# Kernel optimization log

Hardware: AMD Instinct MI355X
Metric: run time of the kernel (lower is better)

The kernel has to match this reference:

```python
import jax, jax.numpy as jnp
import numpy as np

P, Q = 3, 0
DIM = 1 << (P + Q)  # 8 blades, bitmask-indexed: 1,e1,e2,e3,e12,e13,e23,e123
EPS = 1e-6


def _cayley(p, q):
    """Cayley tensor C[i,j,k]: e_i * e_j = sum_k C[i,j,k] e_k for Cl(p,q)."""
    n = p + q
    dim = 1 << n
    C = np.zeros((dim, dim, dim), dtype=np.float32)
    for a in range(dim):
        for b in range(dim):
            # sign from reordering basis vectors into canonical order
            s = 1
            aa = a >> 1
            while aa:
                if bin(aa & b).count('1') & 1:
                    s = -s
                aa >>= 1
            # metric signs from squared shared basis vectors (negative for q part)
            shared = a & b
            for i in range(n):
                if (shared >> i) & 1 and i >= p:
                    s = -s
            C[a, b, a ^ b] = s
    return jnp.asarray(C)

CAYLEY = _cayley(P, Q)
# reversion sign per blade: (-1)^{g(g-1)/2}, g = grade = popcount(bitmask)
REV = jnp.asarray([(-1.0) ** ((bin(k).count('1') * (bin(k).count('1') - 1)) // 2)
                   for k in range(DIM)], dtype=jnp.float32)

B, CH = 131072, 16


def setup_inputs() -> dict:
    key = jax.random.key(0)
    k1, k2, k3 = jax.random.split(key, 3)
    x = jax.random.normal(k1, (B, CH, DIM), dtype=jnp.float32)
    ln_scale = jnp.ones((CH,), dtype=jnp.float32)
    rotor = jax.random.normal(k2, (CH, DIM), dtype=jnp.float32)
    w = jax.random.normal(k3, (CH, CH, DIM), dtype=jnp.float32) / np.sqrt(CH * DIM)
    bias = jnp.zeros((CH, DIM), dtype=jnp.float32)
    return {"x": x, "ln_scale": ln_scale, "rotor": rotor, "w": w, "bias": bias}


def reference(x, ln_scale, rotor, w, bias):
    # CliffordLayerNorm: normalize each channel's multivector by its blade norm
    n = jnp.sqrt(jnp.sum(x * x, axis=-1, keepdims=True) + EPS)  # [B,C,1]
    x = x / n * ln_scale[None, :, None]
    # RotorLayer: unit rotor per channel, sandwich product R x ~R via Cayley
    r = rotor / jnp.sqrt(jnp.sum(rotor * rotor, axis=-1, keepdims=True) + EPS)  # [C,8]
    r_rev = r * REV[None, :]
    t = jnp.einsum('ci,bcj,ijk->bck', r, x, CAYLEY)      # R * x
    x = jnp.einsum('bci,cj,ijk->bck', t, r_rev, CAYLEY)  # (R*x) * ~R
    # GeometricGELU: per-blade exact GELU
    x = jax.nn.gelu(x, approximate=False)
    # CliffordLinear: multivector-valued weights, geometric-product contraction
    out = jnp.einsum('oci,bcj,ijk->bok', w, x, CAYLEY) + bias[None]
    return out
```

## Files before the change

kernel.cpp:

```cpp
#include <hip/hip_runtime.h>
#include <math.h>
#include <stdint.h>

#define CH 16
#define DIM 8
#define ROW 128
#define TILE_ROWS 64
#define BLK 256

typedef __attribute__((ext_vector_type(8))) short bf16x8;
typedef __attribute__((ext_vector_type(4))) float f32x4;
typedef __attribute__((ext_vector_type(4))) unsigned int u32x4;

__device__ __forceinline__ float csign(int a, int b) {
    int s = 0;
    int aa = a >> 1;
    while (aa) { s ^= (__popc(aa & b) & 1); aa >>= 1; }
    return s ? -1.0f : 1.0f;
}

__device__ __forceinline__ unsigned short f2bf(float f) {
    union { float f; unsigned u; } x; x.f = f;
    unsigned r = x.u + 0x7FFF + ((x.u >> 16) & 1);
    return (unsigned short)(r >> 16);
}

__device__ __forceinline__ float gelu_poly(float s) {
    const float z = s * 0.70710678f;
    const float u = z * z;
    float p = -8.5483270e-04f;
    p = fmaf(p, u,  5.2239776e-03f);
    p = fmaf(p, u, -2.6866138e-02f);
    p = fmaf(p, u,  1.1283792e-01f);
    p = fmaf(p, u, -3.7612639e-01f);
    p = fmaf(p, u,  1.1283792e+00f);
    return 0.5f * s * fmaf(z, p, 1.0f);
}

__device__ __forceinline__ void barrier_lgkm() {
    asm volatile("s_waitcnt lgkmcnt(0)" ::: "memory");
    __builtin_amdgcn_s_barrier();
    __builtin_amdgcn_sched_barrier(0);
}

__global__ void precompute_kernel(const float* __restrict__ rotor,
                                  const float* __restrict__ w,
                                  const float* __restrict__ ln_scale,
                                  float* __restrict__ ws)
{
    const int t = threadIdx.x;
    unsigned short* D   = (unsigned short*)ws;
    unsigned short* w2r = D + 16384;

    if (blockIdx.x == 0) {
        ((u32x4*)D)[t]        = (u32x4){0u, 0u, 0u, 0u};
        ((u32x4*)D)[t + 1024] = (u32x4){0u, 0u, 0u, 0u};
        __syncthreads();

        if (t < CH) {
            const int c = t;
            float r[8];
            float nn = 0.f;
            #pragma unroll
            for (int i = 0; i < 8; ++i) { r[i] = rotor[c * 8 + i]; nn += r[i] * r[i]; }
            const float inv = rsqrtf(nn + 1e-6f);
            #pragma unroll
            for (int i = 0; i < 8; ++i) r[i] *= inv;

            const float REVv[8] = {1.f, 1.f, 1.f, -1.f, 1.f, -1.f, -1.f, -1.f};
            float rr[8];
            #pragma unroll
            for (int j = 0; j < 8; ++j) rr[j] = r[j] * REVv[j];

            float L[8][8], R[8][8];
            #pragma unroll
            for (int a = 0; a < 8; ++a)
                #pragma unroll
                for (int b = 0; b < 8; ++b) { L[a][b] = 0.f; R[a][b] = 0.f; }

            #pragma unroll
            for (int i = 0; i < 8; ++i)
                #pragma unroll
                for (int j = 0; j < 8; ++j) {
                    const float s = csign(i, j);
                    L[i ^ j][j] += r[i] * s;
                    R[i ^ j][i] += rr[j] * s;
                }

            const float sc = ln_scale[c];
            #pragma unroll
            for (int k = 0; k < 8; ++k)
                #pragma unroll
                for (int m = 0; m < 8; ++m) {
                    float acc = 0.f;
                    #pragma unroll
                    for (int i = 0; i < 8; ++i) acc += R[k][i] * L[i][m];
                    D[(c * 8 + k) * ROW + (c * 8 + m)] = f2bf(acc * sc);
                }
        }
    } else {
        #pragma unroll
        for (int task = t; task < ROW * CH; task += 1024) {
            const int outf = task >> 4;
            const int ci   = task & 15;
            const int kb = outf & 7, o = outf >> 3;
            const float4 w0 = *(const float4*)(w + (o * CH + ci) * 8);
            const float4 w1 = *(const float4*)(w + (o * CH + ci) * 8 + 4);
            const float wv[8] = {w0.x, w0.y, w0.z, w0.w, w1.x, w1.y, w1.z, w1.w};
            bf16x8 pk;
            #pragma unroll
            for (int j = 0; j < 8; ++j) {
                const int i = kb ^ j;
                pk[j] = (short)f2bf(wv[i] * csign(i, j));
            }
            *(bf16x8*)(w2r + outf * ROW + ci * 8) = pk;
        }
    }
}


__device__ __forceinline__ void phase1_mv(const float4 a, const float4 b,
                                          const bf16x8* Df, unsigned short* sG,
                                          int wave, int lcol, int lkg, int rt) {
    const float nn = a.x*a.x + a.y*a.y + a.z*a.z + a.w*a.w
                   + b.x*b.x + b.y*b.y + b.z*b.z + b.w*b.w;
    const float inv = rsqrtf(nn + 1e-6f);
    bf16x8 af;
    af[0] = (short)f2bf(a.x * inv); af[1] = (short)f2bf(a.y * inv);
    af[2] = (short)f2bf(a.z * inv); af[3] = (short)f2bf(a.w * inv);
    af[4] = (short)f2bf(b.x * inv); af[5] = (short)f2bf(b.y * inv);
    af[6] = (short)f2bf(b.z * inv); af[7] = (short)f2bf(b.w * inv);

    f32x4 p0 = (f32x4){0.f, 0.f, 0.f, 0.f};
    f32x4 p1 = (f32x4){0.f, 0.f, 0.f, 0.f};
    p0 = __builtin_amdgcn_mfma_f32_16x16x32_bf16(af, Df[0], p0, 0, 0, 0);
    p1 = __builtin_amdgcn_mfma_f32_16x16x32_bf16(af, Df[1], p1, 0, 0, 0);

    #pragma unroll
    for (int ctl = 0; ctl < 2; ++ctl) {
        const f32x4 p = ctl ? p1 : p0;
        const int colg = (2 * wave + ctl) * 16 + lcol;
        #pragma unroll
        for (int j = 0; j < 4; ++j) {
            const float y = gelu_poly(p[j]);
            const int row   = rt * 16 + lkg * 4 + j;
            const int chunk = (colg >> 3) ^ (row & 15);
            sG[row * ROW + chunk * 8 + (colg & 7)] = f2bf(y);
        }
    }
}

__global__ __launch_bounds__(BLK, 4) void fused_kernel(
        const float* __restrict__ x,
        const float* __restrict__ bias,
        const float* __restrict__ ws,
        float* __restrict__ out)
{
    __shared__ unsigned short sG[TILE_ROWS * ROW];

    const int t    = threadIdx.x;
    const int lane = t & 63;
    const int wave = t >> 6;
    const int lcol = lane & 15;
    const int lkg  = lane >> 4;
    const int c    = 4 * wave + lkg;

    const unsigned short* D   = (const unsigned short*)ws;
    const unsigned short* w2r = D + 16384;

    const size_t row0 = (size_t)blockIdx.x * TILE_ROWS;

    float4 xa[4], xb[4];
    #pragma unroll
    for (int rt = 0; rt < 4; ++rt) {
        const float4* xp = (const float4*)(x + ((row0 + rt * 16 + lcol) * CH + c) * DIM);
        xa[rt] = xp[0];
        xb[rt] = xp[1];
    }

    bf16x8 Df[2];
    #pragma unroll
    for (int ctl = 0; ctl < 2; ++ctl) {
        const int col = (2 * wave + ctl) * 16 + lcol;
        Df[ctl] = *(const bf16x8*)(D + col * ROW + 32 * wave + lkg * 8);
    }

    #pragma unroll
    for (int rt = 0; rt < 4; ++rt)
        phase1_mv(xa[rt], xb[rt], Df, sG, wave, lcol, lkg, rt);

    const int colb = wave * 32;
    bf16x8 Bf[2][4];
    #pragma unroll
    for (int ct = 0; ct < 2; ++ct)
        #pragma unroll
        for (int ks = 0; ks < 4; ++ks) {
            const int col = colb + ct * 16 + lcol;
            Bf[ct][ks] = *(const bf16x8*)(w2r + col * ROW + ks * 32 + lkg * 8);
        }
    float bv[2];
    bv[0] = bias[colb + lcol];
    bv[1] = bias[colb + 16 + lcol];

    barrier_lgkm();

    f32x4 acc[4][2];
    #pragma unroll
    for (int rt = 0; rt < 4; ++rt)
        #pragma unroll
        for (int ct = 0; ct < 2; ++ct)
            acc[rt][ct] = (f32x4){0.f, 0.f, 0.f, 0.f};

    #pragma unroll
    for (int rt = 0; rt < 4; ++rt) {
        const int row = rt * 16 + lcol;
        #pragma unroll
        for (int ks = 0; ks < 4; ++ks) {
            const int chunk = (ks * 4 + lkg) ^ (row & 15);
            const bf16x8 afr = *(const bf16x8*)(sG + row * ROW + chunk * 8);
            acc[rt][0] = __builtin_amdgcn_mfma_f32_16x16x32_bf16(
                             afr, Bf[0][ks], acc[rt][0], 0, 0, 0);
            acc[rt][1] = __builtin_amdgcn_mfma_f32_16x16x32_bf16(
                             afr, Bf[1][ks], acc[rt][1], 0, 0, 0);
        }
    }

    #pragma unroll
    for (int rt = 0; rt < 4; ++rt) {
        const size_t rbase = row0 + rt * 16 + lkg * 4;
        #pragma unroll
        for (int j = 0; j < 4; ++j) {
            #pragma unroll
            for (int ct = 0; ct < 2; ++ct) {
                const int col = colb + ct * 16 + lcol;
                out[(rbase + j) * ROW + col] = acc[rt][ct][j] + bv[ct];
            }
        }
    }
}

extern "C" void kernel_launch(void* const* d_in, const int* in_sizes, int n_in,
                              void* d_out, int out_size, void* d_ws, size_t ws_size,
                              hipStream_t stream)
{
    const float* x        = (const float*)d_in[0];
    const float* ln_scale = (const float*)d_in[1];
    const float* rotor    = (const float*)d_in[2];
    const float* w        = (const float*)d_in[3];
    const float* bias     = (const float*)d_in[4];
    float* out = (float*)d_out;
    float* ws  = (float*)d_ws;

    precompute_kernel<<<dim3(2), dim3(1024), 0, stream>>>(rotor, w, ln_scale, ws);

    const int nrows   = in_sizes[0] / (CH * DIM);
    const int nblocks = nrows / TILE_ROWS;

    fused_kernel<<<dim3(nblocks), dim3(BLK), 0, stream>>>(x, bias, ws, out);
}
```

Baseline: 36.99 us.

## Give each wave independent row tiles with weights staged in LDS

After: 37.50 us. No clear change (+1.4%).

```diff
diff --git a/kernel.cpp b/kernel.cpp
--- a/kernel.cpp
+++ b/kernel.cpp
@@ -5,8 +5,8 @@
 #define CH 16
 #define DIM 8
 #define ROW 128
-#define TILE_ROWS 64
 #define BLK 256
+#define ROWS_PER_BLOCK 128
 
 typedef __attribute__((ext_vector_type(8))) short bf16x8;
 typedef __attribute__((ext_vector_type(4))) float f32x4;
@@ -37,12 +37,6 @@
     return 0.5f * s * fmaf(z, p, 1.0f);
 }
 
-__device__ __forceinline__ void barrier_lgkm() {
-    asm volatile("s_waitcnt lgkmcnt(0)" ::: "memory");
-    __builtin_amdgcn_s_barrier();
-    __builtin_amdgcn_sched_barrier(0);
-}
-
 __global__ void precompute_kernel(const float* __restrict__ rotor,
                                   const float* __restrict__ w,
                                   const float* __restrict__ ln_scale,
@@ -118,123 +112,119 @@
     }
 }
 
-
-__device__ __forceinline__ void phase1_mv(const float4 a, const float4 b,
-                                          const bf16x8* Df, unsigned short* sG,
-                                          int wave, int lcol, int lkg, int rt) {
-    const float nn = a.x*a.x + a.y*a.y + a.z*a.z + a.w*a.w
-                   + b.x*b.x + b.y*b.y + b.z*b.z + b.w*b.w;
-    const float inv = rsqrtf(nn + 1e-6f);
-    bf16x8 af;
-    af[0] = (short)f2bf(a.x * inv); af[1] = (short)f2bf(a.y * inv);
-    af[2] = (short)f2bf(a.z * inv); af[3] = (short)f2bf(a.w * inv);
-    af[4] = (short)f2bf(b.x * inv); af[5] = (short)f2bf(b.y * inv);
-    af[6] = (short)f2bf(b.z * inv); af[7] = (short)f2bf(b.w * inv);
-
-    f32x4 p0 = (f32x4){0.f, 0.f, 0.f, 0.f};
-    f32x4 p1 = (f32x4){0.f, 0.f, 0.f, 0.f};
-    p0 = __builtin_amdgcn_mfma_f32_16x16x32_bf16(af, Df[0], p0, 0, 0, 0);
-    p1 = __builtin_amdgcn_mfma_f32_16x16x32_bf16(af, Df[1], p1, 0, 0, 0);
-
-    #pragma unroll
-    for (int ctl = 0; ctl < 2; ++ctl) {
-        const f32x4 p = ctl ? p1 : p0;
-        const int colg = (2 * wave + ctl) * 16 + lcol;
-        #pragma unroll
-        for (int j = 0; j < 4; ++j) {
-            const float y = gelu_poly(p[j]);
-            const int row   = rt * 16 + lkg * 4 + j;
-            const int chunk = (colg >> 3) ^ (row & 15);
-            sG[row * ROW + chunk * 8 + (colg & 7)] = f2bf(y);
-        }
-    }
-}
-
 __global__ __launch_bounds__(BLK, 4) void fused_kernel(
         const float* __restrict__ x,
         const float* __restrict__ bias,
         const float* __restrict__ ws,
         float* __restrict__ out)
 {
-    __shared__ unsigned short sG[TILE_ROWS * ROW];
+    __shared__ unsigned short sW[ROW * ROW];
+    __shared__ unsigned short sG[4][16 * ROW];
 
     const int t    = threadIdx.x;
     const int lane = t & 63;
     const int wave = t >> 6;
     const int lcol = lane & 15;
     const int lkg  = lane >> 4;
-    const int c    = 4 * wave + lkg;
 
     const unsigned short* D   = (const unsigned short*)ws;
     const unsigned short* w2r = D + 16384;
 
-    const size_t row0 = (size_t)blockIdx.x * TILE_ROWS;
-
-    float4 xa[4], xb[4];
-    #pragma unroll
-    for (int rt = 0; rt < 4; ++rt) {
-        const float4* xp = (const float4*)(x + ((row0 + rt * 16 + lcol) * CH + c) * DIM);
-        xa[rt] = xp[0];
-        xb[rt] = xp[1];
+    #pragma unroll
+    for (int i = 0; i < 8; ++i) {
+        const int idx   = t + i * BLK;
+        const int col   = idx >> 4;
+        const int ch    = idx & 15;
+        const int chunk = ch ^ (col & 15);
+        const bf16x8 v = *(const bf16x8*)(w2r + col * ROW + ch * 8);
+        *(bf16x8*)(&sW[col * ROW + chunk * 8]) = v;
     }
 
-    bf16x8 Df[2];
-    #pragma unroll
-    for (int ctl = 0; ctl < 2; ++ctl) {
-        const int col = (2 * wave + ctl) * 16 + lcol;
-        Df[ctl] = *(const bf16x8*)(D + col * ROW + 32 * wave + lkg * 8);
-    }
-
-    #pragma unroll
-    for (int rt = 0; rt < 4; ++rt)
-        phase1_mv(xa[rt], xb[rt], Df, sG, wave, lcol, lkg, rt);
-
-    const int colb = wave * 32;
-    bf16x8 Bf[2][4];
-    #pragma unroll
-    for (int ct = 0; ct < 2; ++ct)
+    bf16x8 Df[4][2];
+    #pragma unroll
+    for (int g = 0; g < 4; ++g)
+        #pragma unroll
+        for (int h = 0; h < 2; ++h) {
+            const int col = 32 * g + 16 * h + lcol;
+            Df[g][h] = *(const bf16x8*)(D + col * ROW + 32 * g + lkg * 8);
+        }
+
+    float bv[8];
+    #pragma unroll
+    for (int ct = 0; ct < 8; ++ct) bv[ct] = bias[ct * 16 + lcol];
+
+    __syncthreads();
+
+    unsigned short* mG = &sG[wave][0];
+
+    #pragma unroll
+    for (int tt = 0; tt < 2; ++tt) {
+        const size_t row0 = (size_t)blockIdx.x * ROWS_PER_BLOCK
+                          + (tt * 4 + wave) * 16;
+
+        float4 xa[4], xb[4];
+        #pragma unroll
+        for (int g = 0; g < 4; ++g) {
+            const float4* xp = (const float4*)(x + ((row0 + lcol) * CH + 4 * g + lkg) * DIM);
+            xa[g] = xp[0];
+            xb[g] = xp[1];
+        }
+
+        #pragma unroll
+        for (int g = 0; g < 4; ++g) {
+            const float4 a = xa[g], b = xb[g];
+            const float nn = a.x*a.x + a.y*a.y + a.z*a.z + a.w*a.w
+                           + b.x*b.x + b.y*b.y + b.z*b.z + b.w*b.w;
+            const float inv = rsqrtf(nn + 1e-6f);
+            bf16x8 af;
+            af[0] = (short)f2bf(a.x * inv); af[1] = (short)f2bf(a.y * inv);
+            af[2] = (short)f2bf(a.z * inv); af[3] = (short)f2bf(a.w * inv);
+            af[4] = (short)f2bf(b.x * inv); af[5] = (short)f2bf(b.y * inv);
+            af[6] = (short)f2bf(b.z * inv); af[7] = (short)f2bf(b.w * inv);
+
+            #pragma unroll
+            for (int h = 0; h < 2; ++h) {
+                f32x4 p = (f32x4){0.f, 0.f, 0.f, 0.f};
+                p = __builtin_amdgcn_mfma_f32_16x16x32_bf16(af, Df[g][h], p, 0, 0, 0);
+                const int feat   = 32 * g + 16 * h + lcol;
+                const int chunk0 = feat >> 3;
+                #pragma unroll
+                for (int j = 0; j < 4; ++j) {
+                    const float y = gelu_poly(p[j]);
+                    const int row   = lkg * 4 + j;
+                    const int chunk = chunk0 ^ row;
+                    mG[row * ROW + chunk * 8 + (feat & 7)] = f2bf(y);
+                }
+            }
+        }
+
+        asm volatile("s_waitcnt lgkmcnt(0)" ::: "memory");
+        __builtin_amdgcn_sched_barrier(0);
+
+        f32x4 acc[8];
+        #pragma unroll
+        for (int ct = 0; ct < 8; ++ct) acc[ct] = (f32x4){0.f, 0.f, 0.f, 0.f};
+
         #pragma unroll
         for (int ks = 0; ks < 4; ++ks) {
-            const int col = colb + ct * 16 + lcol;
-            Bf[ct][ks] = *(const bf16x8*)(w2r + col * ROW + ks * 32 + lkg * 8);
-        }
-    float bv[2];
-    bv[0] = bias[colb + lcol];
-    bv[1] = bias[colb + 16 + lcol];
-
-    barrier_lgkm();
-
-    f32x4 acc[4][2];
-    #pragma unroll
-    for (int rt = 0; rt < 4; ++rt)
-        #pragma unroll
-        for (int ct = 0; ct < 2; ++ct)
-            acc[rt][ct] = (f32x4){0.f, 0.f, 0.f, 0.f};
-
-    #pragma unroll
-    for (int rt = 0; rt < 4; ++rt) {
-        const int row = rt * 16 + lcol;
-        #pragma unroll
-        for (int ks = 0; ks < 4; ++ks) {
-            const int chunk = (ks * 4 + lkg) ^ (row & 15);
-            const bf16x8 afr = *(const bf16x8*)(sG + row * ROW + chunk * 8);
-            acc[rt][0] = __builtin_amdgcn_mfma_f32_16x16x32_bf16(
-                             afr, Bf[0][ks], acc[rt][0], 0, 0, 0);
-            acc[rt][1] = __builtin_amdgcn_mfma_f32_16x16x32_bf16(
-                             afr, Bf[1][ks], acc[rt][1], 0, 0, 0);
-        }
-    }
-
-    #pragma unroll
-    for (int rt = 0; rt < 4; ++rt) {
-        const size_t rbase = row0 + rt * 16 + lkg * 4;
+            const int chA = (ks * 4 + lkg) ^ lcol;
+            const bf16x8 afr = *(const bf16x8*)(mG + lcol * ROW + chA * 8);
+            #pragma unroll
+            for (int ct = 0; ct < 8; ++ct) {
+                const int col = ct * 16 + lcol;
+                const int chB = (ks * 4 + lkg) ^ (col & 15);
+                const bf16x8 bfr = *(const bf16x8*)(&sW[col * ROW + chB * 8]);
+                acc[ct] = __builtin_amdgcn_mfma_f32_16x16x32_bf16(
+                              afr, bfr, acc[ct], 0, 0, 0);
+            }
+        }
+
         #pragma unroll
         for (int j = 0; j < 4; ++j) {
-            #pragma unroll
-            for (int ct = 0; ct < 2; ++ct) {
-                const int col = colb + ct * 16 + lcol;
-                out[(rbase + j) * ROW + col] = acc[rt][ct][j] + bv[ct];
-            }
+            const size_t r = row0 + lkg * 4 + j;
+            #pragma unroll
+            for (int ct = 0; ct < 8; ++ct)
+                out[r * ROW + ct * 16 + lcol] = acc[ct][j] + bv[ct];
         }
     }
 }
@@ -254,7 +244,7 @@
     precompute_kernel<<<dim3(2), dim3(1024), 0, stream>>>(rotor, w, ln_scale, ws);
 
     const int nrows   = in_sizes[0] / (CH * DIM);
-    const int nblocks = nrows / TILE_ROWS;
+    const int nblocks = nrows / ROWS_PER_BLOCK;
 
     fused_kernel<<<dim3(nblocks), dim3(BLK), 0, stream>>>(x, bias, ws, out);
 }
```
